# Performance work log

Hardware: AMD Instinct MI355X
Metric: run time of the kernel (lower is better)

## Reference

```python
import jax, jax.numpy as jnp
import numpy as np

B, A, C, G = 8, 65536, 80, 16
TOPK = 50            # pre_anchor_topk
VAR0, VAR1 = 0.1, 0.2  # cfg['variance']
BBOX_T = 0.5
GAMMA = 2.0
ALPHA = 0.5
SL1_W, SL1_BETA = 0.75, 0.11


@jax.custom_vjp
def st_clip(x):
    # Clip.apply: clamp fwd, straight-through bwd
    return jnp.clip(x, 1e-12, None)

def _st_fwd(x):
    return jnp.clip(x, 1e-12, None), None

def _st_bwd(_, g):
    return (g,)

st_clip.defvjp(_st_fwd, _st_bwd)


def point_form(b):  # (cx,cy,w,h) -> (x1,y1,x2,y2)
    return jnp.concatenate([b[..., :2] - b[..., 2:] * 0.5,
                            b[..., :2] + b[..., 2:] * 0.5], axis=-1)


def decode(loc, priors):  # returns center form
    cxcy = priors[..., :2] + loc[..., :2] * VAR0 * priors[..., 2:]
    wh = priors[..., 2:] * jnp.exp(loc[..., 2:] * VAR1)
    return jnp.concatenate([cxcy, wh], axis=-1)


def encode(matched, priors):  # matched: point form, priors: center form
    g_cxcy = ((matched[..., :2] + matched[..., 2:]) * 0.5 - priors[..., :2]) / (VAR0 * priors[..., 2:])
    g_wh = jnp.log((matched[..., 2:] - matched[..., :2]) / priors[..., 2:]) / VAR1
    return jnp.concatenate([g_cxcy, g_wh], axis=-1)


def jaccard(a, b):  # a: [G,4], b: [A,4], point form -> [G,A] IoU
    lt = jnp.maximum(a[:, None, :2], b[None, :, :2])
    rb = jnp.minimum(a[:, None, 2:], b[None, :, 2:])
    wh = jnp.clip(rb - lt, 0.0, None)
    inter = wh[..., 0] * wh[..., 1]
    area_a = (a[:, 2] - a[:, 0]) * (a[:, 3] - a[:, 1])
    area_b = (b[:, 2] - b[:, 0]) * (b[:, 3] - b[:, 1])
    return inter / (area_a[:, None] + area_b[None, :] - inter)


def positive_bag_loss(logits):  # logits: [G, K], bag over K
    w = 1.0 / st_clip(1.0 - logits)
    w = w / jnp.sum(w, axis=1, keepdims=True)
    bag = jnp.sum(w * logits, axis=1)
    return -jnp.log(bag)


def setup_inputs() -> dict:
    key = jax.random.key(0)
    k1, k2, k3, k4, k5, k6 = jax.random.split(key, 6)
    box_regression = jax.random.normal(k1, (B, A, 4), jnp.float32) * 0.1
    cls_logits = jax.random.normal(k2, (B, A, C), jnp.float32) - 2.0
    a_cxcy = jax.random.uniform(k3, (A, 2), jnp.float32, 0.1, 0.9)
    a_wh = jax.random.uniform(k4, (A, 2), jnp.float32, 0.05, 0.3)
    anchors = jnp.concatenate([a_cxcy, a_wh], axis=-1)  # center form
    t_cxcy = jax.random.uniform(k5, (B, G, 2), jnp.float32, 0.2, 0.8)
    t_wh = jax.random.uniform(k6, (B, G, 2), jnp.float32, 0.05, 0.3)
    targets_boxes = jnp.concatenate([t_cxcy - t_wh * 0.5, t_cxcy + t_wh * 0.5], axis=-1)  # point form
    labels = jax.random.randint(jax.random.fold_in(key, 7), (B, G), 0, C)
    return {"box_regression": box_regression, "cls_logits": cls_logits,
            "anchors": anchors, "targets_boxes": targets_boxes, "labels": labels}


def _per_image(box_reg, cls_p, anchors, tboxes, tlabels):
    # ---- box_prob branch (torch: set_grad_enabled(False)) ----
    box_loc = point_form(decode(box_reg, anchors))
    iou = jaccard(tboxes, box_loc)                                  # [G, A]
    t2 = jnp.clip(jnp.max(iou, axis=1, keepdims=True), BBOX_T + 1e-12, None)
    obp = jnp.clip((iou - BBOX_T) / (t2 - BBOX_T), 0.0, 1.0)        # [G, A]
    # sparse per-class scatter + per-class max over objects == segment_max over labels
    seg = jax.ops.segment_max(obp, tlabels, num_segments=C)         # [C, A]
    image_box_prob = jax.lax.stop_gradient(jnp.maximum(seg, 0.0).T)  # [A, C]

    # ---- positive (bag) branch ----
    mqm = jaccard(tboxes, point_form(anchors))                      # [G, A]
    _, matched = jax.lax.top_k(mqm, TOPK)                           # [G, K]
    matched_cls_prob = cls_p[matched, tlabels[:, None]]             # [G, K]
    mot = encode(tboxes[:, None, :], anchors[matched])              # [G, K, 4]
    val = mot - box_reg[matched]
    sl1 = jnp.where(jnp.abs(val) < SL1_BETA,
                    0.5 / SL1_BETA * val * val,
                    jnp.abs(val) - 0.5 * SL1_BETA)
    reg_loss = SL1_W * jnp.sum(sl1, axis=-1)                        # [G, K]
    matched_box_prob = jnp.exp(-reg_loss)
    pos = positive_bag_loss(matched_cls_prob * matched_box_prob)    # [G]
    return pos, image_box_prob


def reference(box_regression, cls_logits, anchors, targets_boxes, labels):
    cls_prob = jax.nn.sigmoid(cls_logits)
    pos, box_prob = jax.vmap(_per_image, in_axes=(0, 0, None, 0, 0))(
        box_regression, cls_prob, anchors, targets_boxes, labels)
    n_pos = B * G
    positive_loss = jnp.sum(pos) / max(1, n_pos)
    x = cls_prob * (1.0 - box_prob)                                 # [B, A, C]
    negative_loss = jnp.sum(x ** GAMMA * -jnp.log(1.0 - x)) / max(1, n_pos * TOPK)
    return positive_loss * ALPHA, negative_loss * (1.0 - ALPHA)
```

## Files before the change

### kernel.cpp

```cpp
#include <hip/hip_runtime.h>
#include <hip/hip_bf16.h>
#include <math.h>

#define BB 8
#define AA 65536
#define CC 80
#define GG 16
#define KK 50
#define NBG (BB*GG)
#define CAP 2048
#define BINS 64
#define NCH 128
#define CHUNK (AA/NCH)
#define NIOU (NCH*BB)
#define NNEG 1024
#define NEGS   262144u
#define NPAIR1 13
#define NPAIR2 7
#define NEG0BASE (26u*NEGS)

#define OFF_ACC   0
#define OFF_T2    16
#define OFF_THR   528
#define OFF_GMASK 1040
#define OFF_CNT   3600
#define OFF_CCNT  4112
#define OFF_HIST  4128
#define HEAD_WORDS 9224
#define HEAD0 1032
#define OFF_CANDV 36896
#define OFF_CANDI 1085472
#define OFF_CLIST 2134048

__global__ void k_pre(unsigned* __restrict__ w, const int* __restrict__ labels,
                      unsigned* __restrict__ gmask){
    int tid=threadIdx.x;
    if (blockIdx.x==0){
        for (int i=tid; i<HEAD0; i+=256) w[i]=0u;
        __syncthreads();
        if (tid<NBG){
            int b=tid>>4; int c=labels[tid];
            atomicOr(&gmask[b*CC+c], 1u<<(tid&15));
        }
    } else {
        for (unsigned i=HEAD0+(blockIdx.x-1)*256u+tid; i<HEAD_WORDS; i+=63u*256u) w[i]=0u;
    }
}

#define NEGF4(v) { \
    float l0=v.x,l1=v.y,l2=v.z,l3=v.w; \
    float e0=__expf(l0), e1=__expf(l1), e2=__expf(l2), e3=__expf(l3); \
    float s0=e0*__builtin_amdgcn_rcpf(1.f+e0); \
    float s1=e1*__builtin_amdgcn_rcpf(1.f+e1); \
    float s2=e2*__builtin_amdgcn_rcpf(1.f+e2); \
    float s3=e3*__builtin_amdgcn_rcpf(1.f+e3); \
    fs+=s0*s0*__logf(1.f+e0); \
    fs+=s1*s1*__logf(1.f+e1); \
    fs+=s2*s2*__logf(1.f+e2); \
    fs+=s3*s3*__logf(1.f+e3); }

__global__ __launch_bounds__(256) void k_iou_neg(const float4* __restrict__ anc4,
        const float4* __restrict__ reg4, const float4* __restrict__ tgt4,
        const float4* __restrict__ lg4,
        unsigned* __restrict__ t2u, unsigned* __restrict__ ghist,
        int* __restrict__ ccnt, unsigned* __restrict__ clist,
        double* __restrict__ acc){
    __shared__ unsigned hist[GG][BINS];
    __shared__ float4 stb[GG];
    __shared__ float sarea[GG];
    __shared__ unsigned st2[GG];
    __shared__ unsigned lbuf[CHUNK];
    __shared__ int lcnt, lbase;
    __shared__ double wsum[4];
    int tid=threadIdx.x;
    int x=blockIdx.x;
    int id=(x>>4)*8+(x&7);

    if (((x>>3)&1)==0){
        double loc=0.0;
        unsigned i0=(unsigned)id*256u+(unsigned)tid;
        for (int gp=0; gp<NPAIR1; ++gp){
            float4 v0=lg4[i0];
            float4 v1=lg4[i0+NEGS];
            i0+=2u*NEGS;
            float fs=0.f;
            NEGF4(v0) NEGF4(v1)
            loc+=(double)fs;
        }
        for (int off=32; off; off>>=1) loc+=__shfl_down(loc,off);
        if ((tid&63)==0) wsum[tid>>6]=loc;
        __syncthreads();
        if (tid==0) atomicAdd(&acc[1],wsum[0]+wsum[1]+wsum[2]+wsum[3]);
        return;
    }

    int blk=id&(NCH-1), b=id>>7;
    for (int j=tid; j<GG*BINS; j+=256) ((unsigned*)hist)[j]=0u;
    if (tid<GG){
        float4 tb=tgt4[b*GG+tid];
        stb[tid]=tb;
        sarea[tid]=(tb.z-tb.x)*(tb.w-tb.y);
        st2[tid]=0u;
    }
    if (tid==0) lcnt=0;
    __syncthreads();
    float mx[GG];
    #pragma unroll
    for (int g=0; g<GG; ++g) mx[g]=0.f;
    int abase=blk*CHUNK+tid;
    for (int it=0; it<CHUNK/256; ++it){
        int a=abase+it*256;
        float4 an=anc4[a];
        float4 br=reg4[b*AA+a];
        float dcx=an.x+br.x*0.1f*an.z;
        float dcy=an.y+br.y*0.1f*an.w;
        float dw=an.z*__expf(br.z*0.2f);
        float dh=an.w*__expf(br.w*0.2f);
        float dx1=dcx-dw*0.5f, dy1=dcy-dh*0.5f, dx2=dcx+dw*0.5f, dy2=dcy+dh*0.5f;
        float dA=dw*dh;
        float ax1=an.x-an.z*0.5f, ay1=an.y-an.w*0.5f;
        float ax2=an.x+an.z*0.5f, ay2=an.y+an.w*0.5f;
        float aA=an.z*an.w;
        bool emit=false;
        #pragma unroll
        for (int g=0; g<GG; ++g){
            float4 tb=stb[g];
            float tA=sarea[g];
            {
                float lx=fmaxf(tb.x,dx1), ly=fmaxf(tb.y,dy1);
                float rx=fminf(tb.z,dx2), ry=fminf(tb.w,dy2);
                float w_=rx-lx, h_=ry-ly;
                if (w_>0.f && h_>0.f){
                    float inter=w_*h_;
                    float iou=inter/(tA+dA-inter);
                    mx[g]=fmaxf(mx[g],iou);
                    if (iou>0.5f) emit=true;
                }
            }
            {
                float lx=fmaxf(tb.x,ax1), ly=fmaxf(tb.y,ay1);
                float rx=fminf(tb.z,ax2), ry=fminf(tb.w,ay2);
                float w_=rx-lx, h_=ry-ly;
                if (w_>0.f && h_>0.f){
                    float inter=w_*h_;
                    float m=inter/(tA+aA-inter);
                    int bin=min(BINS-1,(int)(m*(float)BINS));
                    atomicAdd(&hist[g][bin],1u);
                }
            }
        }
        if (emit){
            int p=atomicAdd(&lcnt,1);
            lbuf[p]=(unsigned)a;
        }
    }
    #pragma unroll
    for (int g=0; g<GG; ++g){
        float v=mx[g];
        for (int off=32; off; off>>=1) v=fmaxf(v,__shfl_down(v,off));
        if ((tid&63)==0) atomicMax(&st2[g],__float_as_uint(v));
    }
    __syncthreads();
    if (tid<GG) atomicMax(&t2u[b*GG+tid],st2[tid]);
    if (tid==0 && lcnt>0) lbase=atomicAdd(ccnt,lcnt);
    __syncthreads();
    for (int j=tid; j<GG*BINS; j+=256){
        unsigned v=((unsigned*)hist)[j];
        if (v) atomicAdd(&ghist[b*GG*BINS+j],v);
    }
    unsigned bb=(unsigned)b<<16;
    for (int j=tid; j<lcnt; j+=256) clist[lbase+j]=bb|lbuf[j];

    {
        double loc=0.0;
        unsigned i0=NEG0BASE+(unsigned)id*256u+(unsigned)tid;
        for (int gp=0; gp<NPAIR2; ++gp){
            float4 v0=lg4[i0];
            float4 v1=lg4[i0+NEGS];
            i0+=2u*NEGS;
            float fs=0.f;
            NEGF4(v0) NEGF4(v1)
            loc+=(double)fs;
        }
        for (int off=32; off; off>>=1) loc+=__shfl_down(loc,off);
        if ((tid&63)==0) wsum[tid>>6]=loc;
        __syncthreads();
        if (tid==0) atomicAdd(&acc[1],wsum[0]+wsum[1]+wsum[2]+wsum[3]);
    }
}

__global__ __launch_bounds__(256) void k_candcorr(const float4* __restrict__ anc4,
        const float4* __restrict__ reg4, const float4* __restrict__ tgt4,
        const float* __restrict__ logits, const unsigned* __restrict__ ghist,
        int* __restrict__ gcnt, float* __restrict__ candv, int* __restrict__ candi,
        const unsigned* __restrict__ gmask, const float* __restrict__ t2f,
        const int* __restrict__ ccnt, const unsigned* __restrict__ clist,
        double* __restrict__ acc){
    __shared__ unsigned hist[GG][BINS];
    __shared__ float4 stb[GG];
    __shared__ float sarea[GG];
    __shared__ float sthr[GG];
    __shared__ double wsum[4];
    int tid=threadIdx.x;
    int x=blockIdx.x;

    if (x>=NIOU){
        int n=*ccnt;
        double loc=0.0;
        for (int i=(x-NIOU)*256+tid; i<n; i+=256*256){
            unsigned key=clist[i];
            int b=key>>16, a=key&0xffff;
            float4 an=anc4[a];
            float4 br=reg4[b*AA+a];
            float dcx=an.x+br.x*0.1f*an.z;
            float dcy=an.y+br.y*0.1f*an.w;
            float dw=an.z*__expf(br.z*0.2f);
            float dh=an.w*__expf(br.w*0.2f);
            float dx1=dcx-dw*0.5f, dy1=dcy-dh*0.5f, dx2=dcx+dw*0.5f, dy2=dcy+dh*0.5f;
            float dA=dw*dh;
            float obp[GG];
            #pragma unroll
            for (int g=0; g<GG; ++g){
                float4 tb=tgt4[b*GG+g];
                float lx=fmaxf(tb.x,dx1), ly=fmaxf(tb.y,dy1);
                float rx=fminf(tb.z,dx2), ry=fminf(tb.w,dy2);
                float w_=fmaxf(rx-lx,0.f), h_=fmaxf(ry-ly,0.f);
                float inter=w_*h_;
                float tA=(tb.z-tb.x)*(tb.w-tb.y);
                float iou=inter/(tA+dA-inter);
                float d=t2f[b*GG+g]-0.5f;
                float inv=(d>0.f)?1.f/d:0.f;
                obp[g]=fminf(fmaxf((iou-0.5f)*inv,0.f),1.f);
            }
            for (int c=0; c<CC; ++c){
                unsigned m=gmask[b*CC+c];
                if (!m) continue;
                float bp=0.f;
                while (m){ unsigned g=(unsigned)__builtin_ctz(m); m&=m-1u; bp=fmaxf(bp,obp[g]); }
                if (bp<=0.f) continue;
                float lg=logits[((size_t)b*AA+(size_t)a)*CC+c];
                float e=__expf(lg);
                float s=e*__builtin_amdgcn_rcpf(1.f+e);
                float xx=s*(1.f-bp);
                float fx=xx*xx*(-__logf(fmaxf(1.f-xx,1e-12f)));
                float fs=s*s*__logf(1.f+e);
                loc+=(double)(fx-fs);
            }
        }
        for (int off=32; off; off>>=1) loc+=__shfl_down(loc,off);
        if ((tid&63)==0) wsum[tid>>6]=loc;
        __syncthreads();
        if (tid==0) atomicAdd(&acc[1],wsum[0]+wsum[1]+wsum[2]+wsum[3]);
        return;
    }

    int blk=x&(NCH-1), b=x>>7;
    int lane=tid&63, wv=tid>>6;
    for (int j=tid; j<GG*BINS; j+=256) ((unsigned*)hist)[j]=ghist[b*GG*BINS+j];
    if (tid<GG){
        float4 tb=tgt4[b*GG+tid];
        stb[tid]=tb;
        sarea[tid]=(tb.z-tb.x)*(tb.w-tb.y);
    }
    __syncthreads();
    #pragma unroll
    for (int gg=0; gg<4; ++gg){
        int g=wv*4+gg;
        unsigned v=hist[g][lane];
        #pragma unroll
        for (int off=1; off<64; off<<=1){
            unsigned o=__shfl_down(v,off);
            if (lane+off<64) v+=o;
        }
        unsigned long long mask=__ballot(v>=KK);
        int bs = mask ? (63-__clzll(mask)) : 0;
        if (lane==0) sthr[g]=(float)bs;
    }
    __syncthreads();
    int abase=blk*CHUNK+tid;
    for (int it=0; it<CHUNK/256; ++it){
        int a=abase+it*256;
        float4 an=anc4[a];
        float ax1=an.x-an.z*0.5f, ay1=an.y-an.w*0.5f;
        float ax2=an.x+an.z*0.5f, ay2=an.y+an.w*0.5f;
        float aA=an.z*an.w;
        #pragma unroll
        for (int g=0; g<GG; ++g){
            float4 tb=stb[g];
            float m=0.f;
            {
                float lx=fmaxf(tb.x,ax1), ly=fmaxf(tb.y,ay1);
                float rx=fminf(tb.z,ax2), ry=fminf(tb.w,ay2);
                float w_=rx-lx, h_=ry-ly;
                if (w_>0.f && h_>0.f){
                    float inter=w_*h_;
                    m=inter/(sarea[g]+aA-inter);
                }
            }
            bool push=(m>0.f && m*(float)BINS>=sthr[g]);
            unsigned long long msk=__ballot(push);
            if (msk){
                int bg=b*GG+g;
                int n=__popcll(msk);
                int ldr=__ffsll((long long)msk)-1;
                int base=0;
                if (lane==ldr) base=atomicAdd(&gcnt[bg],n);
                base=__shfl(base,ldr);
                if (push){
                    int p=base+(int)__popcll(msk&((1ull<<lane)-1ull));
                    if (p<CAP){ candv[bg*CAP+p]=m; candi[bg*CAP+p]=a; }
                }
            }
        }
    }
}

__global__ __launch_bounds__(256) void k_sel(const float4* __restrict__ anc4,
        const float4* __restrict__ reg4, const float4* __restrict__ tgt4,
        const float* __restrict__ logits, const int* __restrict__ labels,
        const int* __restrict__ gcnt, const float* __restrict__ candv,
        const int* __restrict__ candi, double* __restrict__ acc){
    __shared__ float cv[CAP];
    __shared__ int ci[CAP];
    int tid=threadIdx.x;
    int bg=blockIdx.x; int b=bg>>4;
    int cnt=gcnt[bg]; if (cnt>CAP) cnt=CAP;
    for (int j=tid; j<cnt; j+=256){ cv[j]=candv[bg*CAP+j]; ci[j]=candi[bg*CAP+j]; }
    __syncthreads();
    if (tid>=64) return;
    int lane=tid;
    int myA=-1;
    for (int k=0; k<KK; ++k){
        float bv=-1e30f; int bi=0x7fffffff; int bj=-1;
        for (int j=lane; j<cnt; j+=64){
            float v=cv[j]; int ii=ci[j];
            if (v>bv || (v==bv && ii<bi)){ bv=v; bi=ii; bj=j; }
        }
        for (int off=32; off; off>>=1){
            float ov=__shfl_down(bv,off); int oi=__shfl_down(bi,off); int oj=__shfl_down(bj,off);
            if (ov>bv || (ov==bv && oi<bi)){ bv=ov; bi=oi; bj=oj; }
        }
        int wj=__shfl(bj,0); int wi=__shfl(bi,0); float wv=__shfl(bv,0);
        if (wv>-1e29f){
            if (lane==(wj&63)) cv[wj]=-1e30f;
            if (lane==k) myA=wi;
        }
    }
    float p=0.f, u=0.f;
    if (lane<KK && myA>=0){
        float4 tb=tgt4[bg];
        int a=myA;
        float4 an=anc4[a];
        int lab=labels[bg];
        float lg=logits[((size_t)b*AA+(size_t)a)*CC+lab];
        float mcp=1.f/(1.f+expf(-lg));
        float gcx=((tb.x+tb.z)*0.5f-an.x)/(0.1f*an.z);
        float gcy=((tb.y+tb.w)*0.5f-an.y)/(0.1f*an.w);
        float gw=logf((tb.z-tb.x)/an.z)/0.2f;
        float gh=logf((tb.w-tb.y)/an.w)/0.2f;
        float4 br=reg4[b*AA+a];
        float v0=gcx-br.x, v1=gcy-br.y, v2=gw-br.z, v3=gh-br.w;
        float s=0.f;
        {float av=fabsf(v0); s+=(av<0.11f)?4.545454545454546f*v0*v0:av-0.055f;}
        {float av=fabsf(v1); s+=(av<0.11f)?4.545454545454546f*v1*v1:av-0.055f;}
        {float av=fabsf(v2); s+=(av<0.11f)?4.545454545454546f*v2*v2:av-0.055f;}
        {float av=fabsf(v3); s+=(av<0.11f)?4.545454545454546f*v3*v3:av-0.055f;}
        float mbp=expf(-(0.75f*s));
        p=mcp*mbp;
        u=1.f/fmaxf(1.f-p,1e-12f);
    }
    float su=u, sp=u*p;
    for (int off=32; off; off>>=1){ su+=__shfl_down(su,off); sp+=__shfl_down(sp,off); }
    if (lane==0) atomicAdd(&acc[0],(double)(-logf(sp/su)));
}

__global__ void k_fin(const double* __restrict__ acc, float* __restrict__ out){
    out[0]=(float)(0.5*acc[0]/128.0);
    out[1]=(float)(0.5*acc[1]/6400.0);
}

extern "C" void kernel_launch(void* const* d_in, const int* in_sizes, int n_in,
                              void* d_out, int out_size, void* d_ws, size_t ws_size,
                              hipStream_t stream){
    const float4* reg4=(const float4*)d_in[0];
    const float*  logits=(const float*)d_in[1];
    const float4* anc4=(const float4*)d_in[2];
    const float4* tgt4=(const float4*)d_in[3];
    const int*    labels=(const int*)d_in[4];
    char* ws=(char*)d_ws;
    double*   acc   =(double*)(ws+OFF_ACC);
    float*    t2f   =(float*)(ws+OFF_T2);
    unsigned* gmask =(unsigned*)(ws+OFF_GMASK);
    int*      gcnt  =(int*)(ws+OFF_CNT);
    int*      ccnt  =(int*)(ws+OFF_CCNT);
    unsigned* ghist =(unsigned*)(ws+OFF_HIST);
    float*    candv =(float*)(ws+OFF_CANDV);
    int*      candi =(int*)(ws+OFF_CANDI);
    unsigned* clist =(unsigned*)(ws+OFF_CLIST);

    k_pre<<<64,256,0,stream>>>((unsigned*)ws,labels,gmask);
    k_iou_neg<<<NNEG+NIOU,256,0,stream>>>(anc4,reg4,tgt4,(const float4*)logits,
                                          (unsigned*)t2f,ghist,ccnt,clist,acc);
    k_candcorr<<<NIOU+256,256,0,stream>>>(anc4,reg4,tgt4,logits,ghist,gcnt,candv,candi,
                                          gmask,t2f,ccnt,clist,acc);
    k_sel<<<NBG,256,0,stream>>>(anc4,reg4,tgt4,logits,labels,gcnt,candv,candi,acc);
    k_fin<<<1,1,0,stream>>>(acc,(float*)d_out);
}
```

Before: 337.0 us.

## Parallelize top-K selection across four waves and widen correction grid

The top-K selection kernel now splits the candidate list into four slices, and each wave extracts its own top 50. A single wave then merges the 200 survivors into the final top 50, replacing 50 serial passes over up to 2048 candidates by one wave. Separately, the correction-list tail of k_candcorr launches NIOU blocks instead of 256 and uses a matching grid stride, spreading that work over more blocks. The cost is extra shared memory, one more block barrier, and more blocks that may find no work to do.

Result: slower. 384.4 us (+14.0%).

```diff
diff --git a/kernel.cpp b/kernel.cpp
--- a/kernel.cpp
+++ b/kernel.cpp
@@ -207,7 +207,7 @@
     if (x>=NIOU){
         int n=*ccnt;
         double loc=0.0;
-        for (int i=(x-NIOU)*256+tid; i<n; i+=256*256){
+        for (int i=(x-NIOU)*256+tid; i<n; i+=NIOU*256){
             unsigned key=clist[i];
             int b=key>>16, a=key&0xffff;
             float4 an=anc4[a];
@@ -322,29 +322,50 @@
         const int* __restrict__ candi, double* __restrict__ acc){
     __shared__ float cv[CAP];
     __shared__ int ci[CAP];
+    __shared__ float sv[4*KK];
+    __shared__ int si[4*KK];
     int tid=threadIdx.x;
     int bg=blockIdx.x; int b=bg>>4;
     int cnt=gcnt[bg]; if (cnt>CAP) cnt=CAP;
     for (int j=tid; j<cnt; j+=256){ cv[j]=candv[bg*CAP+j]; ci[j]=candi[bg*CAP+j]; }
     __syncthreads();
+    int lane=tid&63, w=tid>>6;
+    {
+        int q=(cnt+3)>>2;
+        int lo=w*q; int hi=lo+q; if (hi>cnt) hi=cnt; if (lo>cnt) lo=cnt;
+        for (int k=0; k<KK; ++k){
+            float bv=-1e30f; int bi=0x7fffffff; int bj=-1;
+            for (int j=lo+lane; j<hi; j+=64){
+                float v=cv[j]; int ii=ci[j];
+                if (v>bv || (v==bv && ii<bi)){ bv=v; bi=ii; bj=j; }
+            }
+            for (int off=32; off; off>>=1){
+                float ov=__shfl_down(bv,off); int oi=__shfl_down(bi,off); int oj=__shfl_down(bj,off);
+                if (ov>bv || (ov==bv && oi<bi)){ bv=ov; bi=oi; bj=oj; }
+            }
+            float wvv=__shfl(bv,0); int wii=__shfl(bi,0); int wjj=__shfl(bj,0);
+            if (lane==0){
+                sv[w*KK+k]=wvv; si[w*KK+k]=wii;
+                if (wvv>-1e29f) cv[wjj]=-1e30f;
+            }
+        }
+    }
+    __syncthreads();
     if (tid>=64) return;
-    int lane=tid;
     int myA=-1;
     for (int k=0; k<KK; ++k){
         float bv=-1e30f; int bi=0x7fffffff; int bj=-1;
-        for (int j=lane; j<cnt; j+=64){
-            float v=cv[j]; int ii=ci[j];
-            if (v>bv || (v==bv && ii<bi)){ bv=v; bi=ii; bj=j; }
+        for (int e=lane; e<4*KK; e+=64){
+            float v=sv[e]; int ii=si[e];
+            if (v>bv || (v==bv && ii<bi)){ bv=v; bi=ii; bj=e; }
         }
         for (int off=32; off; off>>=1){
             float ov=__shfl_down(bv,off); int oi=__shfl_down(bi,off); int oj=__shfl_down(bj,off);
             if (ov>bv || (ov==bv && oi<bi)){ bv=ov; bi=oi; bj=oj; }
         }
-        int wj=__shfl(bj,0); int wi=__shfl(bi,0); float wv=__shfl(bv,0);
-        if (wv>-1e29f){
-            if (lane==(wj&63)) cv[wj]=-1e30f;
-            if (lane==k) myA=wi;
-        }
+        float wvv=__shfl(bv,0); int wii=__shfl(bi,0); int wjj=__shfl(bj,0);
+        if (lane==0 && wvv>-1e29f) sv[wjj]=-1e30f;
+        if (lane==k) myA=(wvv>-1e29f)?wii:-1;
     }
     float p=0.f, u=0.f;
     if (lane<KK && myA>=0){
@@ -401,8 +422,8 @@
     k_pre<<<64,256,0,stream>>>((unsigned*)ws,labels,gmask);
     k_iou_neg<<<NNEG+NIOU,256,0,stream>>>(anc4,reg4,tgt4,(const float4*)logits,
                                           (unsigned*)t2f,ghist,ccnt,clist,acc);
-    k_candcorr<<<NIOU+256,256,0,stream>>>(anc4,reg4,tgt4,logits,ghist,gcnt,candv,candi,
-                                          gmask,t2f,ccnt,clist,acc);
+    k_candcorr<<<NIOU+NIOU,256,0,stream>>>(anc4,reg4,tgt4,logits,ghist,gcnt,candv,candi,
+                                           gmask,t2f,ccnt,clist,acc);
     k_sel<<<NBG,256,0,stream>>>(anc4,reg4,tgt4,logits,labels,gcnt,candv,candi,acc);
     k_fin<<<1,1,0,stream>>>(acc,(float*)d_out);
 }
```
